# Kernel optimization log

Hardware: AMD Instinct MI355X
Metric: run time of the kernel (lower is better)

Reference implementation:

```python
import jax, jax.numpy as jnp
import numpy as np

N, C, RATIO, POS_P = 8192, 5000, 3.0, 0.01


def setup_inputs() -> dict:
    key = jax.random.key(0)
    k1, k2 = jax.random.split(key)
    pred = jax.random.normal(k1, (N, C), dtype=jnp.float32)
    # sparse binary multilabel targets (~50 positives per row)
    target = (jax.random.uniform(k2, (N, C)) < POS_P).astype(jnp.float32)
    return {"pred": pred, "target": target}


def reference(pred, target):
    # pred, target: [N, C]
    num_classes = pred.shape[-1]
    pos = jnp.sum(target, axis=-1)                         # [N] positives per row
    neg = jnp.minimum(pos * RATIO, num_classes - pos)      # [N] hard negatives to keep

    # hard-negative selection: top-neg entries of softmax(pred) - target
    prob = jax.nn.softmax(pred, axis=-1)
    score = prob - target                                  # positives pushed below negatives
    # rank 0 = largest score (matches torch.topk ordering)
    ranks = jnp.argsort(jnp.argsort(-score, axis=-1), axis=-1)
    hard = (ranks < neg[:, None]).astype(pred.dtype)       # [N, C]
    mask = jnp.maximum(target, hard)                       # mask = target.clone(); mask[topk]=1

    # old-torch multilabel_soft_margin_loss(size_average=False) == weighted BCE sum:
    # -(y*log sigmoid(x) + (1-y)*log(1-sigmoid(x))) = softplus(x) - y*x
    bce = jax.nn.softplus(pred) - target * pred
    loss = jnp.sum(mask * bce)
    return loss / jnp.sum(target)
```

## Files before the change

### kernel.cpp

```cpp
#include <hip/hip_runtime.h>
#include <stdint.h>


#define C_DIM 5000
#define C4_DIM 1250
#define BLK 256
#define WSCAP 768
#define CUT 1.25f
#define NSLOT 64

#define WSYNC() asm volatile("s_waitcnt lgkmcnt(0)" ::: "memory")

__device__ __forceinline__ float sp_f(float x) {
    return fmaxf(x, 0.0f) + __logf(1.0f + __expf(-fabsf(x)));
}
__device__ __forceinline__ uint32_t mono_u(float x) {
    uint32_t b = __float_as_uint(x);
    return b ^ ((b & 0x80000000u) ? 0xFFFFFFFFu : 0x80000000u);
}
__device__ __forceinline__ float unmono_f(uint32_t u) {
    uint32_t b = (u & 0x80000000u) ? (u ^ 0x80000000u) : ~u;
    return __uint_as_float(b);
}
__device__ __forceinline__ int vbin_of(float x) {
    int v = (int)((x - CUT) * 128.0f);
    return v > 255 ? 255 : (v < 0 ? 0 : v);
}

__device__ __forceinline__ void find_bin_w(const unsigned int* h, int kp, int lane, int* misc) {
    int c0 = (int)h[4 * lane + 0];
    int c1 = (int)h[4 * lane + 1];
    int c2 = (int)h[4 * lane + 2];
    int c3 = (int)h[4 * lane + 3];
    int lsum = c0 + c1 + c2 + c3;
    int s = lsum;
    #pragma unroll
    for (int off = 1; off < 64; off <<= 1) {
        int o = __shfl_down(s, off);
        if (lane + off < 64) s += o;
    }
    int above = s - lsum;
    if (above < kp && kp <= s) {
        int b, ab;
        if (kp <= above + c3)                { b = 4 * lane + 3; ab = above; }
        else if (kp <= above + c3 + c2)      { b = 4 * lane + 2; ab = above + c3; }
        else if (kp <= above + c3 + c2 + c1) { b = 4 * lane + 1; ab = above + c3 + c2; }
        else                                 { b = 4 * lane;     ab = above + c3 + c2 + c1; }
        misc[0] = b;
        misc[1] = ab;
    }
}

__global__ __launch_bounds__(BLK, 6) void hardneg_kernel(
    const float* __restrict__ pred, const float* __restrict__ target,
    char* __restrict__ ws)
{
    __shared__ uint32_t s_buf[4][WSCAP];
    __shared__ unsigned int s_hist[4][256];
    __shared__ uint32_t s_tiny[4][64];
    __shared__ int s_misc[4][4];

    const int lane = threadIdx.x & 63;
    const int wv = threadIdx.x >> 6;
    const int row = blockIdx.x * 4 + wv;

    uint32_t* sbuf = s_buf[wv];
    unsigned int* h = s_hist[wv];
    int* misc = s_misc[wv];

    const float4* pr4 = (const float4*)(pred + (size_t)row * C_DIM);
    const float4* tg4 = (const float4*)(target + (size_t)row * C_DIM);

    h[lane] = 0; h[lane + 64] = 0; h[lane + 128] = 0; h[lane + 192] = 0;
    WSYNC();

    float acc = 0.0f;
    int pcnt = 0;
    unsigned wcnt = 0;
    const unsigned long long ltmask = (1ull << lane) - 1ull;

    #define PROC(xv, tv) do {                                                  \
        float x_ = (xv);                                                       \
        bool ispos_ = ((tv) != 0.0f);                                          \
        bool cand_ = (!ispos_) && (x_ > CUT);                                  \
        unsigned long long m_ = __ballot(cand_);                               \
        if (cand_) {                                                           \
            unsigned slot_ = wcnt + (unsigned)__popcll(m_ & ltmask);           \
            if (slot_ < WSCAP) sbuf[slot_] = __float_as_uint(x_) ^ 0x80000000u;\
            atomicAdd(&h[vbin_of(x_)], 1u);                                    \
        }                                                                      \
        wcnt += (unsigned)__popcll(m_);                                        \
        if (ispos_) { pcnt++; acc += sp_f(x_) - x_; }                          \
    } while (0)

    #pragma unroll 4
    for (int c = 0; c < 19; ++c) {
        int idx = c * 64 + lane;
        float4 p = pr4[idx];
        float4 t = tg4[idx];
        PROC(p.x, t.x); PROC(p.y, t.y); PROC(p.z, t.z); PROC(p.w, t.w);
    }
    {
        int idx = 19 * 64 + lane;
        float4 p = {0.f, 0.f, 0.f, 0.f}, t = {0.f, 0.f, 0.f, 0.f};
        if (idx < C4_DIM) { p = pr4[idx]; t = tg4[idx]; }
        PROC(p.x, t.x); PROC(p.y, t.y); PROC(p.z, t.z); PROC(p.w, t.w);
    }
    #undef PROC

    int pt = pcnt;
    #pragma unroll
    for (int off = 32; off; off >>= 1) pt += __shfl_xor(pt, off);
    const int pos_total = pt;
    const int k = min(3 * pos_total, C_DIM - pos_total);
    const int cnt = (int)wcnt;
    if (k == 0) return;

    WSYNC();

    uint32_t tu;
    int n_at;
    const bool fb = (k > cnt) || (cnt > WSCAP);

    if (!fb) {
        find_bin_w(h, k, lane, misc);
        WSYNC();
        const int bv = misc[0];
        const int kp = k - misc[1];

        unsigned tcnt = 0;
        const int bound = (cnt + 63) & ~63;
        for (int i = lane; i < bound; i += 64) {
            bool in = (i < cnt);
            uint32_t u = in ? sbuf[i] : 0u;
            bool hit = in && (vbin_of(unmono_f(u)) == bv);
            unsigned long long m = __ballot(hit);
            if (hit) {
                unsigned idx = tcnt + (unsigned)__popcll(m & ltmask);
                if (idx < 64) s_tiny[wv][idx] = u;
            }
            tcnt += (unsigned)__popcll(m);
        }
        WSYNC();

        if (tcnt <= 64) {
            uint32_t ul = (lane < (int)tcnt) ? s_tiny[wv][lane] : 0u;
            int sg = 0, eq = 0;
            for (int j = 0; j < (int)tcnt; ++j) {
                uint32_t uj = (uint32_t)__shfl((int)ul, j);
                sg += (uj > ul);
                eq += (uj == ul);
            }
            if (lane < (int)tcnt && sg < kp && kp <= sg + eq) {
                misc[2] = (int)ul;
                misc[3] = kp - sg;
            }
            WSYNC();
            tu = (uint32_t)misc[2];
            n_at = misc[3];
        } else {
            uint32_t prefix = 0;
            int kq = kp;
            for (int r = 0; r < 4; ++r) {
                const int shift = 24 - 8 * r;
                WSYNC();
                h[lane] = 0; h[lane + 64] = 0; h[lane + 128] = 0; h[lane + 192] = 0;
                WSYNC();
                for (int i = lane; i < cnt; i += 64) {
                    uint32_t u = sbuf[i];
                    bool match = (vbin_of(unmono_f(u)) == bv);
                    if (r > 0) match = match && ((u >> (shift + 8)) == (prefix >> (shift + 8)));
                    if (match) atomicAdd(&h[(u >> shift) & 255u], 1u);
                }
                WSYNC();
                find_bin_w(h, kq, lane, misc);
                WSYNC();
                prefix |= ((uint32_t)misc[0]) << shift;
                kq -= misc[1];
            }
            tu = prefix;
            n_at = kq;
        }

        for (int i = lane; i < cnt; i += 64) {
            uint32_t u = sbuf[i];
            if (u > tu) acc += sp_f(unmono_f(u));
        }
    } else {
        uint32_t prefix = 0;
        int kq = k;
        for (int r = 0; r < 4; ++r) {
            const int shift = 24 - 8 * r;
            WSYNC();
            h[lane] = 0; h[lane + 64] = 0; h[lane + 128] = 0; h[lane + 192] = 0;
            WSYNC();
            for (int i = lane; i < C4_DIM; i += 64) {
                float4 p = pr4[i];
                float4 t = tg4[i];
                float xs[4] = {p.x, p.y, p.z, p.w};
                float tsv[4] = {t.x, t.y, t.z, t.w};
                #pragma unroll
                for (int j = 0; j < 4; ++j) {
                    if (tsv[j] == 0.0f) {
                        uint32_t u = mono_u(xs[j]);
                        bool m = (r == 0) || ((u >> (shift + 8)) == (prefix >> (shift + 8)));
                        if (m) atomicAdd(&h[(u >> shift) & 255u], 1u);
                    }
                }
            }
            WSYNC();
            find_bin_w(h, kq, lane, misc);
            WSYNC();
            prefix |= ((uint32_t)misc[0]) << shift;
            kq -= misc[1];
        }
        tu = prefix;
        n_at = kq;
        for (int i = lane; i < C4_DIM; i += 64) {
            float4 p = pr4[i];
            float4 t = tg4[i];
            float xs[4] = {p.x, p.y, p.z, p.w};
            float tsv[4] = {t.x, t.y, t.z, t.w};
            #pragma unroll
            for (int j = 0; j < 4; ++j) {
                if (tsv[j] == 0.0f && mono_u(xs[j]) > tu) acc += sp_f(xs[j]);
            }
        }
    }

    #pragma unroll
    for (int off = 32; off; off >>= 1) acc += __shfl_down(acc, off);
    if (lane == 0) {
        float rowsum = acc + (float)n_at * sp_f(unmono_f(tu));
        char* slot = ws + (size_t)(row & (NSLOT - 1)) * 16;
        atomicAdd((double*)slot, (double)rowsum);
        atomicAdd((float*)(slot + 8), (float)pos_total);
    }
}

__global__ void hardneg_finalize(const char* __restrict__ ws, float* __restrict__ out)
{
    const int l = threadIdx.x;
    double n = *(const double*)(ws + (size_t)l * 16);
    float d = *(const float*)(ws + (size_t)l * 16 + 8);
    #pragma unroll
    for (int off = 32; off; off >>= 1) {
        n += __shfl_down(n, off);
        d += __shfl_down(d, off);
    }
    if (l == 0) out[0] = (d > 0.0f) ? (float)(n / (double)d) : 0.0f;
}

extern "C" void kernel_launch(void* const* d_in, const int* in_sizes, int n_in,
                              void* d_out, int out_size, void* d_ws, size_t ws_size,
                              hipStream_t stream) {
    const float* pred = (const float*)d_in[0];
    const float* target = (const float*)d_in[1];
    float* out = (float*)d_out;
    char* ws = (char*)d_ws;

    hipMemsetAsync(ws, 0, NSLOT * 16, stream);

    const int nrows = in_sizes[0] / C_DIM;
    hardneg_kernel<<<nrows / 4, BLK, 0, stream>>>(pred, target, ws);
    hardneg_finalize<<<1, 64, 0, stream>>>(ws, out);
}
```

Measured before the change: 351.8 us.

## Double-buffer row streaming through LDS with async global-to-LDS loads

The first pass over each row now uses async global_load_lds copies into per-wave double-buffered LDS tiles, issued two tiles ahead, so memory latency overlaps the candidate and histogram processing. The tail of each row is processed first from registers. Occupancy hint drops from 6 to 3 blocks per CU because of the extra LDS. The atomic accumulation slots are also doubled and padded to 32 bytes to cut contention, with finalize summing both halves.

```diff
diff --git a/kernel.cpp b/kernel.cpp
--- a/kernel.cpp
+++ b/kernel.cpp
@@ -7,9 +7,18 @@
 #define BLK 256
 #define WSCAP 768
 #define CUT 1.25f
-#define NSLOT 64
-
-#define WSYNC() asm volatile("s_waitcnt lgkmcnt(0)" ::: "memory")
+#define NSLOT 128
+#define TILE_F 512
+#define NTILE 9
+
+#define WSYNC()  asm volatile("s_waitcnt lgkmcnt(0)" ::: "memory")
+#define CFENCE() asm volatile("" ::: "memory")
+
+__device__ __forceinline__ void gload16(const void* g, void* l) {
+    __builtin_amdgcn_global_load_lds(
+        (const __attribute__((address_space(1))) void*)g,
+        (__attribute__((address_space(3))) void*)l, 16, 0, 0);
+}
 
 __device__ __forceinline__ float sp_f(float x) {
     return fmaxf(x, 0.0f) + __logf(1.0f + __expf(-fabsf(x)));
@@ -51,10 +60,12 @@
     }
 }
 
-__global__ __launch_bounds__(BLK, 6) void hardneg_kernel(
+__global__ __launch_bounds__(BLK, 3) void hardneg_kernel(
     const float* __restrict__ pred, const float* __restrict__ target,
     char* __restrict__ ws)
 {
+    __shared__ float s_tileP[4][2][TILE_F];
+    __shared__ float s_tileT[4][2][TILE_F];
     __shared__ uint32_t s_buf[4][WSCAP];
     __shared__ unsigned int s_hist[4][256];
     __shared__ uint32_t s_tiny[4][64];
@@ -93,18 +104,46 @@
         if (ispos_) { pcnt++; acc += sp_f(x_) - x_; }                          \
     } while (0)
 
-    #pragma unroll 4
-    for (int c = 0; c < 19; ++c) {
-        int idx = c * 64 + lane;
-        float4 p = pr4[idx];
-        float4 t = tg4[idx];
+    {
+        int i0 = NTILE * (TILE_F / 4) + lane;
+        float4 p = pr4[i0];
+        float4 t = tg4[i0];
         PROC(p.x, t.x); PROC(p.y, t.y); PROC(p.z, t.z); PROC(p.w, t.w);
-    }
-    {
-        int idx = 19 * 64 + lane;
-        float4 p = {0.f, 0.f, 0.f, 0.f}, t = {0.f, 0.f, 0.f, 0.f};
-        if (idx < C4_DIM) { p = pr4[idx]; t = tg4[idx]; }
-        PROC(p.x, t.x); PROC(p.y, t.y); PROC(p.z, t.z); PROC(p.w, t.w);
+        int i1 = i0 + 64;
+        float4 q = {0.f, 0.f, 0.f, 0.f}, s = {0.f, 0.f, 0.f, 0.f};
+        if (i1 < C4_DIM) { q = pr4[i1]; s = tg4[i1]; }
+        PROC(q.x, s.x); PROC(q.y, s.y); PROC(q.z, s.z); PROC(q.w, s.w);
+    }
+    asm volatile("s_waitcnt vmcnt(0)" ::: "memory");
+    __builtin_amdgcn_sched_barrier(0);
+
+    auto issue_tile = [&](int t) {
+        const char* gp = (const char*)(pr4 + (size_t)t * (TILE_F / 4));
+        const char* gt = (const char*)(tg4 + (size_t)t * (TILE_F / 4));
+        char* lp = (char*)&s_tileP[wv][t & 1][0];
+        char* lt = (char*)&s_tileT[wv][t & 1][0];
+        gload16(gp + (size_t)lane * 16,        lp);
+        gload16(gp + 1024 + (size_t)lane * 16, lp + 1024);
+        gload16(gt + (size_t)lane * 16,        lt);
+        gload16(gt + 1024 + (size_t)lane * 16, lt + 1024);
+    };
+
+    issue_tile(0);
+    issue_tile(1);
+    for (int t = 0; t < NTILE; ++t) {
+        if (t < NTILE - 1) { asm volatile("s_waitcnt vmcnt(4)" ::: "memory"); }
+        else               { asm volatile("s_waitcnt vmcnt(0)" ::: "memory"); }
+        __builtin_amdgcn_sched_barrier(0);
+        {
+            const float4* bp = (const float4*)&s_tileP[wv][t & 1][0];
+            const float4* bt = (const float4*)&s_tileT[wv][t & 1][0];
+            float4 p0 = bp[lane],      t0 = bt[lane];
+            float4 p1 = bp[lane + 64], t1 = bt[lane + 64];
+            PROC(p0.x, t0.x); PROC(p0.y, t0.y); PROC(p0.z, t0.z); PROC(p0.w, t0.w);
+            PROC(p1.x, t1.x); PROC(p1.y, t1.y); PROC(p1.z, t1.z); PROC(p1.w, t1.w);
+        }
+        CFENCE();
+        if (t + 2 < NTILE) issue_tile(t + 2);
     }
     #undef PROC
 
@@ -232,7 +271,7 @@
     for (int off = 32; off; off >>= 1) acc += __shfl_down(acc, off);
     if (lane == 0) {
         float rowsum = acc + (float)n_at * sp_f(unmono_f(tu));
-        char* slot = ws + (size_t)(row & (NSLOT - 1)) * 16;
+        char* slot = ws + (size_t)(row & (NSLOT - 1)) * 32;
         atomicAdd((double*)slot, (double)rowsum);
         atomicAdd((float*)(slot + 8), (float)pos_total);
     }
@@ -241,8 +280,14 @@
 __global__ void hardneg_finalize(const char* __restrict__ ws, float* __restrict__ out)
 {
     const int l = threadIdx.x;
-    double n = *(const double*)(ws + (size_t)l * 16);
-    float d = *(const float*)(ws + (size_t)l * 16 + 8);
+    double n = 0.0;
+    float d = 0.0f;
+    #pragma unroll
+    for (int s = 0; s < NSLOT / 64; ++s) {
+        const char* slot = ws + (size_t)(s * 64 + l) * 32;
+        n += *(const double*)slot;
+        d += *(const float*)(slot + 8);
+    }
     #pragma unroll
     for (int off = 32; off; off >>= 1) {
         n += __shfl_down(n, off);
@@ -259,7 +304,7 @@
     float* out = (float*)d_out;
     char* ws = (char*)d_ws;
 
-    hipMemsetAsync(ws, 0, NSLOT * 16, stream);
+    hipMemsetAsync(ws, 0, NSLOT * 32, stream);
 
     const int nrows = in_sizes[0] / C_DIM;
     hardneg_kernel<<<nrows / 4, BLK, 0, stream>>>(pred, target, ws);
```

New measurement: 346.2 us. About the same (-1.6%).
